# Kernel tuning notes

Hardware: AMD Instinct MI355X
Metric: run time of the kernel (lower is better)

The kernel has to match this reference:

```python
import jax, jax.numpy as jnp
import numpy as np
import math

N_NODES = 100000
N_EDGES = 1600000
IN_CH = 128
EDGE_DIM = 8
HEADS = 4
C1, C2 = 10, 5  # per-head out channels of conv1/conv2
N_GRAPHS = 64


def setup_inputs() -> dict:
    key = jax.random.key(0)
    k = jax.random.split(key, 26)
    s = 0.05
    d1, d2 = HEADS * C1, HEADS * C2  # 40, 20
    lin = lambda kk, fi, fo: jax.random.normal(kk, (fi, fo), jnp.float32) * s
    inp = {}
    inp['x'] = jax.random.normal(k[0], (N_NODES, IN_CH), jnp.float32)
    inp['edge_index'] = jax.random.randint(k[1], (2, N_EDGES), 0, N_NODES)
    inp['edge_attr'] = jax.random.normal(k[2], (N_EDGES, EDGE_DIM), jnp.float32)
    inp['batch'] = jnp.sort(jax.random.randint(k[3], (N_NODES,), 0, N_GRAPHS))
    # conv1 params (TransformerConv: lin_query/key/value + lin_edge(no bias) + lin_skip)
    inp['Wq1'] = lin(k[4], IN_CH, d1); inp['bq1'] = jnp.zeros((d1,), jnp.float32)
    inp['Wk1'] = lin(k[5], IN_CH, d1); inp['bk1'] = jnp.zeros((d1,), jnp.float32)
    inp['Wv1'] = lin(k[6], IN_CH, d1); inp['bv1'] = jnp.zeros((d1,), jnp.float32)
    inp['We1'] = lin(k[7], EDGE_DIM, d1)
    inp['Ws1'] = lin(k[8], IN_CH, d1); inp['bs1'] = jnp.zeros((d1,), jnp.float32)
    # conv2 params
    inp['Wq2'] = lin(k[9], d1, d2); inp['bq2'] = jnp.zeros((d2,), jnp.float32)
    inp['Wk2'] = lin(k[10], d1, d2); inp['bk2'] = jnp.zeros((d2,), jnp.float32)
    inp['Wv2'] = lin(k[11], d1, d2); inp['bv2'] = jnp.zeros((d2,), jnp.float32)
    inp['We2'] = lin(k[12], EDGE_DIM, d2)
    inp['Ws2'] = lin(k[13], d1, d2); inp['bs2'] = jnp.zeros((d2,), jnp.float32)
    # MLP head
    inp['W1'] = lin(k[14], d2, 10); inp['b1'] = jnp.zeros((10,), jnp.float32)
    inp['W2'] = lin(k[15], 10, 3); inp['b2'] = jnp.zeros((3,), jnp.float32)
    return inp


def _segment_softmax(alpha, dst, n):
    # numerically stable softmax over incoming edges of each target node
    amax = jax.ops.segment_max(alpha, dst, num_segments=n)
    ex = jnp.exp(alpha - amax[dst])
    den = jax.ops.segment_sum(ex, dst, num_segments=n)
    return ex / (den[dst] + 1e-16)


def _transformer_conv(x, src, dst, eattr, Wq, bq, Wk, bk, Wv, bv, We, Ws, bs, heads, ch):
    n = x.shape[0]
    q = (x @ Wq + bq).reshape(n, heads, ch)
    k = (x @ Wk + bk).reshape(n, heads, ch)
    v = (x @ Wv + bv).reshape(n, heads, ch)
    e = (eattr @ We).reshape(-1, heads, ch)          # [E,H,C]
    kj = k[src] + e                                   # gather + edge bias
    alpha = jnp.einsum('ehc,ehc->eh', q[dst], kj) / math.sqrt(ch)
    alpha = _segment_softmax(alpha, dst, n)           # [E,H]
    msg = (v[src] + e) * alpha[:, :, None]
    out = jax.ops.segment_sum(msg, dst, num_segments=n).reshape(n, heads * ch)
    return out + x @ Ws + bs                          # root/skip connection (beta=False)


def reference(x, edge_index, edge_attr, batch, Wq1, bq1, Wk1, bk1, Wv1, bv1, We1, Ws1, bs1, Wq2, bq2, Wk2, bk2, Wv2, bv2, We2, Ws2, bs2, W1, b1, W2, b2):
    src, dst = edge_index[0], edge_index[1]
    h = jax.nn.relu(_transformer_conv(x, src, dst, edge_attr, Wq1, bq1, Wk1, bk1, Wv1, bv1, We1, Ws1, bs1, HEADS, C1))
    h = jax.nn.relu(_transformer_conv(h, src, dst, edge_attr, Wq2, bq2, Wk2, bk2, Wv2, bv2, We2, Ws2, bs2, HEADS, C2))
    # global_mean_pool
    sums = jax.ops.segment_sum(h, batch, num_segments=N_GRAPHS)
    cnt = jax.ops.segment_sum(jnp.ones((h.shape[0],), h.dtype), batch, num_segments=N_GRAPHS)
    pooled = sums / jnp.maximum(cnt, 1.0)[:, None]
    h = jax.nn.relu(pooled @ W1 + b1)
    return h @ W2 + b2
```

## Files before the change

### kernel.cpp

```cpp
#include <hip/hip_runtime.h>
#include <math.h>

typedef short bf16x8 __attribute__((ext_vector_type(8)));
typedef float f32x4 __attribute__((ext_vector_type(4)));

__device__ __forceinline__ unsigned bfr_(float f) {
    unsigned u = __float_as_uint(f);
    return (u + 0x7fffu + ((u >> 16) & 1u)) >> 16;
}
__device__ __forceinline__ unsigned pack2_(float lo, float hi) {
    return bfr_(lo) | (bfr_(hi) << 16);
}
__device__ __forceinline__ float unlo_(unsigned u) { return __uint_as_float(u << 16); }
__device__ __forceinline__ float unhi_(unsigned u) { return __uint_as_float(u & 0xffff0000u); }
__device__ __forceinline__ float bf2f_(unsigned short us) {
    return __uint_as_float((unsigned)us << 16);
}

__global__ void k_hist(const int* __restrict__ dst, int* __restrict__ deg, int E) {
    int e = blockIdx.x * 256 + threadIdx.x;
    if (e < E) atomicAdd(&deg[dst[e]], 1);
}

__global__ void k_scan1(const int* __restrict__ deg, int* __restrict__ rp,
                        int* __restrict__ bsum, int n) {
    __shared__ int sh[256];
    int t = threadIdx.x;
    int base = blockIdx.x * 1024 + t * 4;
    int v0 = (base + 0 < n) ? deg[base + 0] : 0;
    int v1 = (base + 1 < n) ? deg[base + 1] : 0;
    int v2 = (base + 2 < n) ? deg[base + 2] : 0;
    int v3 = (base + 3 < n) ? deg[base + 3] : 0;
    int ts = v0 + v1 + v2 + v3;
    sh[t] = ts;
    __syncthreads();
    for (int off = 1; off < 256; off <<= 1) {
        int x = (t >= off) ? sh[t - off] : 0;
        __syncthreads();
        sh[t] += x;
        __syncthreads();
    }
    int run = sh[t] - ts;
    if (base + 0 < n) rp[base + 0] = run;
    run += v0;
    if (base + 1 < n) rp[base + 1] = run;
    run += v1;
    if (base + 2 < n) rp[base + 2] = run;
    run += v2;
    if (base + 3 < n) rp[base + 3] = run;
    if (t == 255) bsum[blockIdx.x] = sh[255];
}

__global__ void k_scan2(int* __restrict__ bsum, int nb) {
    __shared__ int sh[256];
    int t = threadIdx.x;
    int v = (t < nb) ? bsum[t] : 0;
    sh[t] = v;
    __syncthreads();
    for (int off = 1; off < 256; off <<= 1) {
        int x = (t >= off) ? sh[t - off] : 0;
        __syncthreads();
        sh[t] += x;
        __syncthreads();
    }
    if (t < nb) bsum[t] = sh[t] - v;
}

__global__ void k_scan3(int* __restrict__ rp, const int* __restrict__ bsum,
                        int* __restrict__ cur, int n, int total) {
    int t = threadIdx.x;
    int base = blockIdx.x * 1024 + t * 4;
    int add = bsum[blockIdx.x];
    if (base + 0 < n) { rp[base + 0] += add; cur[base + 0] = 0; }
    if (base + 1 < n) { rp[base + 1] += add; cur[base + 1] = 0; }
    if (base + 2 < n) { rp[base + 2] += add; cur[base + 2] = 0; }
    if (base + 3 < n) { rp[base + 3] += add; cur[base + 3] = 0; }
    if (blockIdx.x == 0 && t == 0) rp[n] = total;
}

__global__ void k_scatter(const int* __restrict__ src, const int* __restrict__ dst,
                          const int* __restrict__ rp, int* __restrict__ cur,
                          const float4* __restrict__ ea, int* __restrict__ src_perm,
                          uint4* __restrict__ eap, int E) {
    int e = blockIdx.x * 256 + threadIdx.x;
    if (e >= E) return;
    float4 a = ea[(size_t)e * 2 + 0];
    float4 b = ea[(size_t)e * 2 + 1];
    uint4 u;
    u.x = pack2_(a.x, a.y);
    u.y = pack2_(a.z, a.w);
    u.z = pack2_(b.x, b.y);
    u.w = pack2_(b.z, b.w);
    int d = dst[e];
    int pos = rp[d] + atomicAdd(&cur[d], 1);
    src_perm[pos] = src[e];
    eap[pos] = u;
}

__global__ void k_wprep(const float* __restrict__ Wq, const float* __restrict__ Wk,
                        const float* __restrict__ Wv, const float* __restrict__ Ws,
                        short* __restrict__ wpackT) {
    int i = blockIdx.x * 256 + threadIdx.x;
    if (i >= 160 * 136) return;
    int c = i / 136, k = i % 136;
    short v = 0;
    if (k < 128) {
        const float* W = c < 40 ? Wq : c < 80 ? Wk : c < 120 ? Wv : Ws;
        v = (short)bfr_(W[k * 40 + (c % 40)]);
    }
    wpackT[i] = v;
}

__global__ __launch_bounds__(256) void k_proj1m(
    const float* __restrict__ X, const short* __restrict__ wpackT,
    const float* __restrict__ bq, const float* __restrict__ bk,
    const float* __restrict__ bv, const float* __restrict__ bs,
    float* __restrict__ qO, unsigned* __restrict__ kvO,
    unsigned short* __restrict__ sO, int N) {
    __shared__ short xs[64 * 136];
    __shared__ short wt[160 * 136];
    int t = threadIdx.x;
    int nb = blockIdx.x * 64;
    for (int i = t; i < 64 * 32; i += 256) {
        int nl = i >> 5, k4 = (i & 31) * 4;
        int node = nb + nl;
        float4 val = make_float4(0.f, 0.f, 0.f, 0.f);
        if (node < N) val = *(const float4*)(X + (size_t)node * 128 + k4);
        uint2 pk;
        pk.x = pack2_(val.x, val.y);
        pk.y = pack2_(val.z, val.w);
        *(uint2*)(xs + nl * 136 + k4) = pk;
    }
    {
        const uint4* wsrc = (const uint4*)wpackT;
        uint4* wdst = (uint4*)wt;
        for (int i = t; i < 2720; i += 256) wdst[i] = wsrc[i];
    }
    __syncthreads();
    int wv = t >> 6;
    int lane = t & 63;
    int lrow = lane & 15;
    int kgrp = lane >> 4;
    bf16x8 afr[4];
    const short* xbase = xs + (wv * 16 + lrow) * 136;
#pragma unroll
    for (int kk = 0; kk < 4; ++kk)
        afr[kk] = *(const bf16x8*)(xbase + kk * 32 + kgrp * 8);
    f32x4 acc[10];
#pragma unroll
    for (int nt = 0; nt < 10; ++nt) acc[nt] = (f32x4){0.f, 0.f, 0.f, 0.f};
#pragma unroll
    for (int nt = 0; nt < 10; ++nt) {
        const short* wbase = wt + (nt * 16 + lrow) * 136;
#pragma unroll
        for (int kk = 0; kk < 4; ++kk) {
            bf16x8 bfr8 = *(const bf16x8*)(wbase + kk * 32 + kgrp * 8);
            acc[nt] = __builtin_amdgcn_mfma_f32_16x16x32_bf16(afr[kk], bfr8, acc[nt],
                                                              0, 0, 0);
        }
    }
    __syncthreads();
    float* cs = (float*)wt;
#pragma unroll
    for (int nt = 0; nt < 10; ++nt)
#pragma unroll
        for (int r = 0; r < 4; ++r)
            cs[(wv * 16 + kgrp * 4 + r) * 160 + nt * 16 + lrow] = acc[nt][r];
    __syncthreads();
    for (int i = t; i < 64 * 40; i += 256) {
        int nl = i / 40, c = i % 40;
        int node = nb + nl;
        if (node < N) {
            const float* row = cs + nl * 160;
            float qv = row[c] + bq[c];
            float kf = row[40 + c] + bk[c];
            float vf = row[80 + c] + bv[c];
            float sv = row[120 + c] + bs[c];
            qO[(size_t)node * 40 + c] = qv;
            kvO[(size_t)node * 40 + c] = pack2_(kf, vf);
            sO[(size_t)node * 40 + c] = (unsigned short)bfr_(sv);
        }
    }
}

template <int FIN, int CH, int KTILE, int NPT, int CHPAD, int NPB>
__global__ __launch_bounds__(256) void k_proj(
    const float* __restrict__ X,
    const float* __restrict__ Wq, const float* __restrict__ Wk,
    const float* __restrict__ Wv, const float* __restrict__ Ws,
    const float* __restrict__ bq, const float* __restrict__ bk,
    const float* __restrict__ bv, const float* __restrict__ bs,
    float* __restrict__ qO, unsigned* __restrict__ kvO,
    unsigned short* __restrict__ sO, int N) {
    constexpr int FOUT = 4 * CH;
    constexpr int STRIDE = 4 * CHPAD;
    constexpr int COLS = 4 * FOUT;
    constexpr int NCG = COLS / 10;
    constexpr int NG = 256 / NCG;
    static_assert(NG * NPT == NPB, "geometry");
    constexpr int F4 = FIN / 4;
    __shared__ float xs[FIN * NPB];
    __shared__ float wbuf[KTILE * COLS];
    int t = threadIdx.x;
    int nb = blockIdx.x * NPB;
    for (int i = t; i < NPB * F4; i += 256) {
        int nl = i % NPB;
        int k4 = (i / NPB) * 4;
        int node = nb + nl;
        float4 val = make_float4(0.f, 0.f, 0.f, 0.f);
        if (node < N) val = *(const float4*)(X + (size_t)node * FIN + k4);
        xs[(k4 + 0) * NPB + nl] = val.x;
        xs[(k4 + 1) * NPB + nl] = val.y;
        xs[(k4 + 2) * NPB + nl] = val.z;
        xs[(k4 + 3) * NPB + nl] = val.w;
    }
    int cg = t % NCG, ng = t / NCG;
    int which = (cg * 10) / FOUT, cc0 = (cg * 10) % FOUT;
    float acc[NPT][10];
#pragma unroll
    for (int i = 0; i < NPT; ++i)
#pragma unroll
        for (int j = 0; j < 10; ++j) acc[i][j] = 0.f;

    for (int kt = 0; kt < FIN; kt += KTILE) {
        __syncthreads();
        for (int i = t; i < KTILE * (COLS / 4); i += 256) {
            int kk = i / (COLS / 4);
            int c4 = (i % (COLS / 4)) * 4;
            int wh = c4 / FOUT, cc = c4 % FOUT;
            const float* Wsrc = wh == 0 ? Wq : wh == 1 ? Wk : wh == 2 ? Wv : Ws;
            float4 wv = *(const float4*)(Wsrc + (size_t)(kt + kk) * FOUT + cc);
            wbuf[kk * COLS + c4 + 0] = wv.x;
            wbuf[kk * COLS + c4 + 1] = wv.y;
            wbuf[kk * COLS + c4 + 2] = wv.z;
            wbuf[kk * COLS + c4 + 3] = wv.w;
        }
        __syncthreads();
#pragma unroll 4
        for (int kk = 0; kk < KTILE; ++kk) {
            float xv[NPT];
            if constexpr (NPT == 4) {
                float4 x4 = *(const float4*)(xs + (kt + kk) * NPB + ng * 4);
                xv[0] = x4.x; xv[1] = x4.y; xv[2] = x4.z; xv[3] = x4.w;
            } else if constexpr (NPT == 2) {
                float2 x2 = *(const float2*)(xs + (kt + kk) * NPB + ng * 2);
                xv[0] = x2.x; xv[1] = x2.y;
            } else {
                xv[0] = xs[(kt + kk) * NPB + ng];
            }
            const float2* wp = (const float2*)(wbuf + kk * COLS + cg * 10);
            float wv[10];
#pragma unroll
            for (int jj = 0; jj < 5; ++jj) {
                float2 w2 = wp[jj];
                wv[2 * jj] = w2.x;
                wv[2 * jj + 1] = w2.y;
            }
#pragma unroll
            for (int i = 0; i < NPT; ++i)
#pragma unroll
                for (int j = 0; j < 10; ++j) acc[i][j] += xv[i] * wv[j];
        }
    }
    const float* B = which == 0 ? bq : which == 1 ? bk : which == 2 ? bv : bs;
    float bias[10];
#pragma unroll
    for (int j = 0; j < 10; ++j) bias[j] = B[cc0 + j];
    __syncthreads();
    if (which == 0) {
#pragma unroll
        for (int i = 0; i < NPT; ++i) {
            int node = nb + ng * NPT + i;
            if (node < N)
#pragma unroll
                for (int j = 0; j < 10; ++j) {
                    int col = cc0 + j, hh = col / CH, cc = col % CH;
                    qO[(size_t)node * STRIDE + hh * CHPAD + cc] = acc[i][j] + bias[j];
                }
        }
    } else if (which == 3) {
#pragma unroll
        for (int i = 0; i < NPT; ++i) {
            int node = nb + ng * NPT + i;
            if (node < N)
#pragma unroll
                for (int j = 0; j < 10; ++j)
                    sO[(size_t)node * FOUT + cc0 + j] =
                        (unsigned short)bfr_(acc[i][j] + bias[j]);
        }
    } else if (which == 1) {
#pragma unroll
        for (int i = 0; i < NPT; ++i) {
            int nl = ng * NPT + i;
#pragma unroll
            for (int j = 0; j < 10; ++j) wbuf[nl * FOUT + cc0 + j] = acc[i][j] + bias[j];
        }
    }
    __syncthreads();
    if (which == 2) {
#pragma unroll
        for (int i = 0; i < NPT; ++i) {
            int nl = ng * NPT + i;
            int node = nb + nl;
            if (node < N)
#pragma unroll
                for (int j = 0; j < 10; ++j) {
                    int col = cc0 + j, hh = col / CH, cc = col % CH;
                    float kf = wbuf[nl * FOUT + cc0 + j];
                    kvO[(size_t)node * STRIDE + hh * CHPAD + cc] =
                        pack2_(kf, acc[i][j] + bias[j]);
                }
        }
    }
}

template <int CH, int CHPAD, bool SHIFT>
__global__ __launch_bounds__(256) void k_conv(
    const int* __restrict__ rp, const int* __restrict__ src_perm,
    const uint4* __restrict__ eap, const float* __restrict__ We,
    const float* __restrict__ q, const unsigned* __restrict__ kv,
    const unsigned short* __restrict__ skp, float* __restrict__ hout,
    float inv_sqrt, int N) {
    constexpr int D = 4 * CH;
    constexpr int STRIDE = 4 * CHPAD;
    constexpr int RAWN = SHIFT ? CHPAD + 2 : CHPAD;
    constexpr int NLD = RAWN / 4;
    __shared__ float we_s[8 * D];
    for (int i = threadIdx.x; i < 8 * D; i += 256) we_s[i] = We[i];
    __syncthreads();
    int g = blockIdx.x * 256 + threadIdx.x;
    int node = g >> 4;
    int h = g & 3;
    int qtr = (g >> 2) & 3;
    if (node >= N) return;
    int start_off = SHIFT ? ((h * CH) & ~3) : h * CHPAD;
    int rs = rp[node], re = rp[node + 1];
    float qh[CH];
    {
        float qraw[RAWN];
        const float4* qp = (const float4*)(q + (size_t)node * STRIDE + start_off);
#pragma unroll
        for (int i = 0; i < NLD; ++i) *(float4*)&qraw[4 * i] = qp[i];
        if constexpr (SHIFT) {
            if (h & 1) {
#pragma unroll
                for (int c = 0; c < CH; ++c) qraw[c] = qraw[c + 2];
            }
        }
#pragma unroll
        for (int c = 0; c < CH; ++c) qh[c] = qraw[c];
    }
    float qe[8];
#pragma unroll
    for (int j = 0; j < 8; ++j) {
        float sE = 0.f;
#pragma unroll
        for (int c = 0; c < CH; ++c) sE += qh[c] * we_s[j * D + h * CH + c];
        qe[j] = sE;
    }
    float m = -3.0e38f, l = 0.f;
    float accv[CH] = {};
    float acce[8] = {};
    for (int p = rs + qtr; p < re; p += 4) {
        int sidx = src_perm[p];
        uint4 eu = eap[p];
        float ea8[8];
        ea8[0] = unlo_(eu.x); ea8[1] = unhi_(eu.x);
        ea8[2] = unlo_(eu.y); ea8[3] = unhi_(eu.y);
        ea8[4] = unlo_(eu.z); ea8[5] = unhi_(eu.z);
        ea8[6] = unlo_(eu.w); ea8[7] = unhi_(eu.w);
        unsigned kraw[RAWN];
        const uint4* kp = (const uint4*)(kv + (size_t)sidx * STRIDE + start_off);
#pragma unroll
        for (int i = 0; i < NLD; ++i) *(uint4*)&kraw[4 * i] = kp[i];
        if constexpr (SHIFT) {
            if (h & 1) {
#pragma unroll
                for (int c = 0; c < CH; ++c) kraw[c] = kraw[c + 2];
            }
        }
        float a = 0.f;
        float vj[CH];
#pragma unroll
        for (int c = 0; c < CH; ++c) {
            unsigned u = kraw[c];
            a += qh[c] * unlo_(u);
            vj[c] = unhi_(u);
        }
#pragma unroll
        for (int j = 0; j < 8; ++j) a += qe[j] * ea8[j];
        a *= inv_sqrt;
        float mn = fmaxf(m, a);
        float so = __expf(m - mn);
        float w = __expf(a - mn);
        l = l * so + w;
#pragma unroll
        for (int c = 0; c < CH; ++c) accv[c] = accv[c] * so + w * vj[c];
#pragma unroll
        for (int j = 0; j < 8; ++j) acce[j] = acce[j] * so + w * ea8[j];
        m = mn;
    }
#pragma unroll
    for (int mask = 4; mask <= 8; mask <<= 1) {
        float mo = __shfl_xor(m, mask);
        float lo = __shfl_xor(l, mask);
        float mn = fmaxf(m, mo);
        float s1 = (m > -1e37f) ? __expf(m - mn) : 0.f;
        float s2 = (mo > -1e37f) ? __expf(mo - mn) : 0.f;
        l = l * s1 + lo * s2;
#pragma unroll
        for (int c = 0; c < CH; ++c) {
            float ao = __shfl_xor(accv[c], mask);
            accv[c] = accv[c] * s1 + ao * s2;
        }
#pragma unroll
        for (int j = 0; j < 8; ++j) {
            float ao = __shfl_xor(acce[j], mask);
            acce[j] = acce[j] * s1 + ao * s2;
        }
        m = mn;
    }
    if (qtr == 0) {
        float inv = 1.0f / (l + 1e-16f);
#pragma unroll
        for (int c = 0; c < CH; ++c) {
            float ec = 0.f;
#pragma unroll
            for (int j = 0; j < 8; ++j) ec += acce[j] * we_s[j * D + h * CH + c];
            float o = (accv[c] + ec) * inv + bf2f_(skp[(size_t)node * D + h * CH + c]);
            hout[(size_t)node * D + h * CH + c] = fmaxf(o, 0.f);
        }
    }
}

__global__ void k_pool(const float* __restrict__ h2, const int* __restrict__ batch,
                       float* __restrict__ pooled, float* __restrict__ cnt, int N) {
    int t = blockIdx.x * 256 + threadIdx.x;
    int start = t * 16;
    if (start >= N) return;
    int end = min(start + 16, N);
    float acc[20];
#pragma unroll
    for (int c = 0; c < 20; ++c) acc[c] = 0.f;
    int cg = batch[start];
    float run = 0.f;
    for (int n = start; n < end; ++n) {
        int g = batch[n];
        if (g != cg) {
#pragma unroll
            for (int c = 0; c < 20; ++c) atomicAdd(&pooled[cg * 20 + c], acc[c]);
            atomicAdd(&cnt[cg], run);
#pragma unroll
            for (int c = 0; c < 20; ++c) acc[c] = 0.f;
            run = 0.f;
            cg = g;
        }
#pragma unroll
        for (int c = 0; c < 20; ++c) acc[c] += h2[(size_t)n * 20 + c];
        run += 1.f;
    }
#pragma unroll
    for (int c = 0; c < 20; ++c) atomicAdd(&pooled[cg * 20 + c], acc[c]);
    atomicAdd(&cnt[cg], run);
}

__global__ void k_mlp(const float* __restrict__ pooled, const float* __restrict__ cnt,
                      const float* __restrict__ W1, const float* __restrict__ b1,
                      const float* __restrict__ W2, const float* __restrict__ b2,
                      float* __restrict__ out) {
    int g = threadIdx.x;
    if (g >= 64) return;
    float ic = 1.0f / fmaxf(cnt[g], 1.0f);
    float p[20];
#pragma unroll
    for (int i = 0; i < 20; ++i) p[i] = pooled[g * 20 + i] * ic;
    float hid[10];
#pragma unroll
    for (int j = 0; j < 10; ++j) {
        float a = b1[j];
#pragma unroll
        for (int i = 0; i < 20; ++i) a += p[i] * W1[i * 10 + j];
        hid[j] = fmaxf(a, 0.f);
    }
#pragma unroll
    for (int o = 0; o < 3; ++o) {
        float a = b2[o];
#pragma unroll
        for (int j = 0; j < 10; ++j) a += hid[j] * W2[j * 3 + o];
        out[g * 3 + o] = a;
    }
}

extern "C" void kernel_launch(void* const* d_in, const int* in_sizes, int n_in,
                              void* d_out, int out_size, void* d_ws, size_t ws_size,
                              hipStream_t stream) {
    const float* x   = (const float*)d_in[0];
    const int* ei    = (const int*)d_in[1];
    const float* ea  = (const float*)d_in[2];
    const int* batch = (const int*)d_in[3];
    const float *Wq1 = (const float*)d_in[4],  *bq1 = (const float*)d_in[5];
    const float *Wk1 = (const float*)d_in[6],  *bk1 = (const float*)d_in[7];
    const float *Wv1 = (const float*)d_in[8],  *bv1 = (const float*)d_in[9];
    const float *We1 = (const float*)d_in[10];
    const float *Ws1 = (const float*)d_in[11], *bs1 = (const float*)d_in[12];
    const float *Wq2 = (const float*)d_in[13], *bq2 = (const float*)d_in[14];
    const float *Wk2 = (const float*)d_in[15], *bk2 = (const float*)d_in[16];
    const float *Wv2 = (const float*)d_in[17], *bv2 = (const float*)d_in[18];
    const float *We2 = (const float*)d_in[19];
    const float *Ws2 = (const float*)d_in[20], *bs2 = (const float*)d_in[21];
    const float *W1  = (const float*)d_in[22], *b1  = (const float*)d_in[23];
    const float *W2  = (const float*)d_in[24], *b2  = (const float*)d_in[25];

    const int N = in_sizes[0] / 128;
    const int E = in_sizes[1] / 2;
    const int* srcI = ei;
    const int* dstI = ei + E;

    float* F = (float*)d_ws;
    float*          q    = F;
    unsigned*       kv   = (unsigned*)(F + 4000000);
    float*          h1   = F + 8000000;
    float*          h2   = F + 8000000;
    unsigned short* s_bf = (unsigned short*)(F + 12000000);
    uint4*          eap  = (uint4*)(F + 14000000);
    int*       src_perm  = (int*)(F + 20400000);
    int* I = (int*)(F + 22000000);
    int* deg  = I;
    int* cur  = I;
    int* rpR  = I + 100352;
    int* bsum = I + 200704;
    short* wpackT = (short*)(F + 22250000);
    float* pooled = F + 22300000;
    float* cnt    = pooled + 1280;

    const int SCAN_BLOCKS = (N + 1023) / 1024;
    const int EB = (E + 255) / 256;

    hipMemsetAsync(deg, 0, (size_t)N * 4, stream);
    hipMemsetAsync(pooled, 0, (1280 + 64) * 4, stream);

    k_wprep<<<(160 * 136 + 255) / 256, 256, 0, stream>>>(Wq1, Wk1, Wv1, Ws1, wpackT);
    k_hist<<<EB, 256, 0, stream>>>(dstI, deg, E);
    k_scan1<<<SCAN_BLOCKS, 256, 0, stream>>>(deg, rpR, bsum, N);
    k_scan2<<<1, 256, 0, stream>>>(bsum, SCAN_BLOCKS);
    k_scan3<<<SCAN_BLOCKS, 256, 0, stream>>>(rpR, bsum, cur, N, E);
    k_scatter<<<EB, 256, 0, stream>>>(srcI, dstI, rpR, cur, (const float4*)ea,
                                      src_perm, eap, E);

    k_proj1m<<<(N + 63) / 64, 256, 0, stream>>>(x, wpackT, bq1, bk1, bv1, bs1,
                                                q, kv, s_bf, N);
    k_conv<10, 10, true><<<(16 * N + 255) / 256, 256, 0, stream>>>(
        rpR, src_perm, eap, We1, q, kv, s_bf, h1, 0.31622776601683794f, N);

    k_proj<40, 5, 40, 1, 8, 32><<<(N + 31) / 32, 256, 0, stream>>>(
        h1, Wq2, Wk2, Wv2, Ws2, bq2, bk2, bv2, bs2, q, kv, s_bf, N);
    k_conv<5, 8, false><<<(16 * N + 255) / 256, 256, 0, stream>>>(
        rpR, src_perm, eap, We2, q, kv, s_bf, h2, 0.4472135954999579f, N);

    k_pool<<<((N + 15) / 16 + 255) / 256, 256, 0, stream>>>(h2, batch, pooled, cnt, N);
    k_mlp<<<1, 64, 0, stream>>>(pooled, cnt, W1, b1, W2, b2, (float*)d_out);
}
```

Measured before the change: 475.2 us.

## Pad per-head KV to aligned rows, store q in bf16, partition edge scatter

Conv1 K/V rows are now padded to 16 entries per head (64 per node) so each head starts on an aligned boundary, which removes the shift/realign logic in the gather loop. Q is stored as bf16 with per-head padding, which halves the query read. The edge scatter now launches 8 passes, and each pass handles only the edges whose destination falls in one eighth of the CSR range. This is meant to localise scattered writes for better cache behaviour, at the cost of reading dst and rp eight times. The padded kv layout for conv1 raises gather bytes per edge (64 vs 40 words per node), trading bandwidth for alignment.

```diff
diff --git a/kernel.cpp b/kernel.cpp
--- a/kernel.cpp
+++ b/kernel.cpp
@@ -78,12 +78,17 @@
     if (blockIdx.x == 0 && t == 0) rp[n] = total;
 }
 
-__global__ void k_scatter(const int* __restrict__ src, const int* __restrict__ dst,
-                          const int* __restrict__ rp, int* __restrict__ cur,
-                          const float4* __restrict__ ea, int* __restrict__ src_perm,
-                          uint4* __restrict__ eap, int E) {
-    int e = blockIdx.x * 256 + threadIdx.x;
+__global__ void k_scatter8(const int* __restrict__ src, const int* __restrict__ dst,
+                           const int* __restrict__ rp, int* __restrict__ cur,
+                           const float4* __restrict__ ea, int* __restrict__ src_perm,
+                           uint4* __restrict__ eap, int E) {
+    int p = blockIdx.x & 7;
+    int e = (blockIdx.x >> 3) * 256 + threadIdx.x;
     if (e >= E) return;
+    int d = dst[e];
+    int pos0 = rp[d];
+    int q = (int)(((long long)pos0 * 8) / E);
+    if (q != p) return;
     float4 a = ea[(size_t)e * 2 + 0];
     float4 b = ea[(size_t)e * 2 + 1];
     uint4 u;
@@ -91,8 +96,7 @@
     u.y = pack2_(a.z, a.w);
     u.z = pack2_(b.x, b.y);
     u.w = pack2_(b.z, b.w);
-    int d = dst[e];
-    int pos = rp[d] + atomicAdd(&cur[d], 1);
+    int pos = pos0 + atomicAdd(&cur[d], 1);
     src_perm[pos] = src[e];
     eap[pos] = u;
 }
@@ -115,7 +119,7 @@
     const float* __restrict__ X, const short* __restrict__ wpackT,
     const float* __restrict__ bq, const float* __restrict__ bk,
     const float* __restrict__ bv, const float* __restrict__ bs,
-    float* __restrict__ qO, unsigned* __restrict__ kvO,
+    unsigned short* __restrict__ qO, unsigned* __restrict__ kvO,
     unsigned short* __restrict__ sO, int N) {
     __shared__ short xs[64 * 136];
     __shared__ short wt[160 * 136];
@@ -172,28 +176,28 @@
         int node = nb + nl;
         if (node < N) {
             const float* row = cs + nl * 160;
+            int hh = c / 10, cc = c % 10;
             float qv = row[c] + bq[c];
             float kf = row[40 + c] + bk[c];
             float vf = row[80 + c] + bv[c];
             float sv = row[120 + c] + bs[c];
-            qO[(size_t)node * 40 + c] = qv;
-            kvO[(size_t)node * 40 + c] = pack2_(kf, vf);
+            qO[(size_t)node * 64 + hh * 16 + cc] = (unsigned short)bfr_(qv);
+            kvO[(size_t)node * 64 + hh * 16 + cc] = pack2_(kf, vf);
             sO[(size_t)node * 40 + c] = (unsigned short)bfr_(sv);
         }
     }
 }
 
-template <int FIN, int CH, int KTILE, int NPT, int CHPAD, int NPB>
+template <int FIN, int CH, int KTILE, int NPT, int KVP, int QP, int NPB>
 __global__ __launch_bounds__(256) void k_proj(
     const float* __restrict__ X,
     const float* __restrict__ Wq, const float* __restrict__ Wk,
     const float* __restrict__ Wv, const float* __restrict__ Ws,
     const float* __restrict__ bq, const float* __restrict__ bk,
     const float* __restrict__ bv, const float* __restrict__ bs,
-    float* __restrict__ qO, unsigned* __restrict__ kvO,
+    unsigned short* __restrict__ qO, unsigned* __restrict__ kvO,
     unsigned short* __restrict__ sO, int N) {
     constexpr int FOUT = 4 * CH;
-    constexpr int STRIDE = 4 * CHPAD;
     constexpr int COLS = 4 * FOUT;
     constexpr int NCG = COLS / 10;
     constexpr int NG = 256 / NCG;
@@ -275,7 +279,8 @@
 #pragma unroll
                 for (int j = 0; j < 10; ++j) {
                     int col = cc0 + j, hh = col / CH, cc = col % CH;
-                    qO[(size_t)node * STRIDE + hh * CHPAD + cc] = acc[i][j] + bias[j];
+                    qO[(size_t)node * 4 * QP + hh * QP + cc] =
+                        (unsigned short)bfr_(acc[i][j] + bias[j]);
                 }
         }
     } else if (which == 3) {
@@ -307,24 +312,23 @@
                 for (int j = 0; j < 10; ++j) {
                     int col = cc0 + j, hh = col / CH, cc = col % CH;
                     float kf = wbuf[nl * FOUT + cc0 + j];
-                    kvO[(size_t)node * STRIDE + hh * CHPAD + cc] =
+                    kvO[(size_t)node * 4 * KVP + hh * KVP + cc] =
                         pack2_(kf, acc[i][j] + bias[j]);
                 }
         }
     }
 }
 
-template <int CH, int CHPAD, bool SHIFT>
+template <int CH, int KVP, int QP>
 __global__ __launch_bounds__(256) void k_conv(
     const int* __restrict__ rp, const int* __restrict__ src_perm,
     const uint4* __restrict__ eap, const float* __restrict__ We,
-    const float* __restrict__ q, const unsigned* __restrict__ kv,
+    const unsigned short* __restrict__ qbf, const unsigned* __restrict__ kv,
     const unsigned short* __restrict__ skp, float* __restrict__ hout,
     float inv_sqrt, int N) {
     constexpr int D = 4 * CH;
-    constexpr int STRIDE = 4 * CHPAD;
-    constexpr int RAWN = SHIFT ? CHPAD + 2 : CHPAD;
-    constexpr int NLD = RAWN / 4;
+    constexpr int NQL = (QP * 2) / 16;
+    constexpr int NKL = KVP / 4;
     __shared__ float we_s[8 * D];
     for (int i = threadIdx.x; i < 8 * D; i += 256) we_s[i] = We[i];
     __syncthreads();
@@ -333,23 +337,16 @@
     int h = g & 3;
     int qtr = (g >> 2) & 3;
     if (node >= N) return;
-    int start_off = SHIFT ? ((h * CH) & ~3) : h * CHPAD;
     int rs = rp[node], re = rp[node + 1];
+    unsigned short q16[8 * NQL];
+    {
+        const uint4* qp = (const uint4*)(qbf + (size_t)node * 4 * QP + h * QP);
+#pragma unroll
+        for (int i = 0; i < NQL; ++i) *(uint4*)&q16[8 * i] = qp[i];
+    }
     float qh[CH];
-    {
-        float qraw[RAWN];
-        const float4* qp = (const float4*)(q + (size_t)node * STRIDE + start_off);
-#pragma unroll
-        for (int i = 0; i < NLD; ++i) *(float4*)&qraw[4 * i] = qp[i];
-        if constexpr (SHIFT) {
-            if (h & 1) {
-#pragma unroll
-                for (int c = 0; c < CH; ++c) qraw[c] = qraw[c + 2];
-            }
-        }
-#pragma unroll
-        for (int c = 0; c < CH; ++c) qh[c] = qraw[c];
-    }
+#pragma unroll
+    for (int c = 0; c < CH; ++c) qh[c] = bf2f_(q16[c]);
     float qe[8];
 #pragma unroll
     for (int j = 0; j < 8; ++j) {
@@ -369,16 +366,10 @@
         ea8[2] = unlo_(eu.y); ea8[3] = unhi_(eu.y);
         ea8[4] = unlo_(eu.z); ea8[5] = unhi_(eu.z);
         ea8[6] = unlo_(eu.w); ea8[7] = unhi_(eu.w);
-        unsigned kraw[RAWN];
-        const uint4* kp = (const uint4*)(kv + (size_t)sidx * STRIDE + start_off);
-#pragma unroll
-        for (int i = 0; i < NLD; ++i) *(uint4*)&kraw[4 * i] = kp[i];
-        if constexpr (SHIFT) {
-            if (h & 1) {
-#pragma unroll
-                for (int c = 0; c < CH; ++c) kraw[c] = kraw[c + 2];
-            }
-        }
+        unsigned kraw[4 * NKL];
+        const uint4* kp = (const uint4*)(kv + (size_t)sidx * 4 * KVP + h * KVP);
+#pragma unroll
+        for (int i = 0; i < NKL; ++i) *(uint4*)&kraw[4 * i] = kp[i];
         float a = 0.f;
         float vj[CH];
 #pragma unroll
@@ -517,20 +508,20 @@
     const int* dstI = ei + E;
 
     float* F = (float*)d_ws;
-    float*          q    = F;
-    unsigned*       kv   = (unsigned*)(F + 4000000);
-    float*          h1   = F + 8000000;
-    float*          h2   = F + 8000000;
-    unsigned short* s_bf = (unsigned short*)(F + 12000000);
-    uint4*          eap  = (uint4*)(F + 14000000);
-    int*       src_perm  = (int*)(F + 20400000);
-    int* I = (int*)(F + 22000000);
+    unsigned short* qbf = (unsigned short*)F;
+    unsigned*       kv  = (unsigned*)(F + 3200000);
+    float*          h1  = F + 9600000;
+    float*          h2  = F + 9600000;
+    unsigned short* s_bf = (unsigned short*)(F + 13600000);
+    uint4*          eap = (uint4*)(F + 15600000);
+    int*       src_perm = (int*)(F + 22000000);
+    int* I = (int*)(F + 23600000);
     int* deg  = I;
     int* cur  = I;
     int* rpR  = I + 100352;
     int* bsum = I + 200704;
-    short* wpackT = (short*)(F + 22250000);
-    float* pooled = F + 22300000;
+    short* wpackT = (short*)(F + 23900000);
+    float* pooled = F + 23950000;
     float* cnt    = pooled + 1280;
 
     const int SCAN_BLOCKS = (N + 1023) / 1024;
@@ -544,18 +535,18 @@
     k_scan1<<<SCAN_BLOCKS, 256, 0, stream>>>(deg, rpR, bsum, N);
     k_scan2<<<1, 256, 0, stream>>>(bsum, SCAN_BLOCKS);
     k_scan3<<<SCAN_BLOCKS, 256, 0, stream>>>(rpR, bsum, cur, N, E);
-    k_scatter<<<EB, 256, 0, stream>>>(srcI, dstI, rpR, cur, (const float4*)ea,
-                                      src_perm, eap, E);
+    k_scatter8<<<EB * 8, 256, 0, stream>>>(srcI, dstI, rpR, cur, (const float4*)ea,
+                                           src_perm, eap, E);
 
     k_proj1m<<<(N + 63) / 64, 256, 0, stream>>>(x, wpackT, bq1, bk1, bv1, bs1,
-                                                q, kv, s_bf, N);
-    k_conv<10, 10, true><<<(16 * N + 255) / 256, 256, 0, stream>>>(
-        rpR, src_perm, eap, We1, q, kv, s_bf, h1, 0.31622776601683794f, N);
-
-    k_proj<40, 5, 40, 1, 8, 32><<<(N + 31) / 32, 256, 0, stream>>>(
-        h1, Wq2, Wk2, Wv2, Ws2, bq2, bk2, bv2, bs2, q, kv, s_bf, N);
-    k_conv<5, 8, false><<<(16 * N + 255) / 256, 256, 0, stream>>>(
-        rpR, src_perm, eap, We2, q, kv, s_bf, h2, 0.4472135954999579f, N);
+                                                qbf, kv, s_bf, N);
+    k_conv<10, 16, 16><<<(16 * N + 255) / 256, 256, 0, stream>>>(
+        rpR, src_perm, eap, We1, qbf, kv, s_bf, h1, 0.31622776601683794f, N);
+
+    k_proj<40, 5, 40, 1, 8, 8, 32><<<(N + 31) / 32, 256, 0, stream>>>(
+        h1, Wq2, Wk2, Wv2, Ws2, bq2, bk2, bv2, bs2, qbf, kv, s_bf, N);
+    k_conv<5, 8, 8><<<(16 * N + 255) / 256, 256, 0, stream>>>(
+        rpR, src_perm, eap, We2, qbf, kv, s_bf, h2, 0.4472135954999579f, N);
 
     k_pool<<<((N + 15) / 16 + 255) / 256, 256, 0, stream>>>(h2, batch, pooled, cnt, N);
     k_mlp<<<1, 64, 0, stream>>>(pooled, cnt, W1, b1, W2, b2, (float*)d_out);
```

After: 480.4 us. Within noise of the previous version (+1.1%).
